# Optimization experiments

Hardware: AMD Instinct MI355X
Metric: run time of the kernel (lower is better)

The kernel has to match this reference:

```python
import jax, jax.numpy as jnp
import numpy as np

EMBED_DIM = 768
NUM_HEADS = 12
HEAD_DIM = EMBED_DIM // NUM_HEADS


def setup_inputs() -> dict:
    key = jax.random.key(0)
    ks = jax.random.split(key, 6)
    B, N = 8, 1024
    x = jax.random.normal(ks[0], (B, N, EMBED_DIM), dtype=jnp.float32)
    pos_embedding = jax.random.normal(ks[1], (1, NUM_HEADS, N, N), dtype=jnp.float32)
    s_in = 1.0 / np.sqrt(EMBED_DIM)
    W_qkv = jax.random.normal(ks[2], (EMBED_DIM, 3 * EMBED_DIM), dtype=jnp.float32) * s_in
    b_qkv = jnp.zeros((3 * EMBED_DIM,), dtype=jnp.float32)
    W_proj = jax.random.normal(ks[3], (EMBED_DIM, EMBED_DIM), dtype=jnp.float32) * s_in
    b_proj = jnp.zeros((EMBED_DIM,), dtype=jnp.float32)
    return {"x": x, "pos_embedding": pos_embedding, "W_qkv": W_qkv,
            "b_qkv": b_qkv, "W_proj": W_proj, "b_proj": b_proj}


def reference(x, pos_embedding, W_qkv, b_qkv, W_proj, b_proj):
    B, N, C = x.shape
    H, D = NUM_HEADS, HEAD_DIM
    qkv = x @ W_qkv + b_qkv                      # [B,N,3C]
    qkv = qkv.reshape(B, N, 3, H, D)
    q = qkv[:, :, 0].transpose(0, 2, 1, 3)       # [B,H,N,D]
    k = qkv[:, :, 1].transpose(0, 2, 1, 3)
    v = qkv[:, :, 2].transpose(0, 2, 1, 3)
    # NOTE: bias is added BEFORE scaling, matching the original module.
    scores = (jnp.einsum('bhnd,bhmd->bhnm', q, k) + pos_embedding) / jnp.sqrt(
        jnp.asarray(D, dtype=x.dtype))
    attn = jax.nn.softmax(scores, axis=-1)       # dropout is identity in eval
    out = jnp.einsum('bhnm,bhmd->bhnd', attn, v)
    out = out.transpose(0, 2, 1, 3).reshape(B, N, C)
    return out @ W_proj + b_proj
```

## Files before the change

kernel.cpp:

```cpp
#include <hip/hip_runtime.h>

#define SEQ   1024
#define HEADS 12
#define CDIM  768
#define BATCH 8

#define QSCALE 0.18033688011112042f

typedef __attribute__((ext_vector_type(8))) short bf16x8;
typedef __attribute__((ext_vector_type(4))) float f32x4;
typedef __attribute__((ext_vector_type(16))) float f32x16;
typedef __attribute__((ext_vector_type(4))) float float4v;
typedef __attribute__((ext_vector_type(4))) short short4v;

__device__ __forceinline__ void gload_lds16(const void* g, void* l) {
  __builtin_amdgcn_global_load_lds(
      (const __attribute__((address_space(1))) unsigned int*)g,
      (__attribute__((address_space(3))) unsigned int*)l, 16, 0, 0);
}

__device__ __forceinline__ unsigned short f2bf(float f) {
  union { float f; unsigned u; } v; v.f = f;
  unsigned r = v.u + 0x7fff + ((v.u >> 16) & 1);
  return (unsigned short)(r >> 16);
}

__device__ __forceinline__ unsigned cvtpk(float a, float b) {
  unsigned r;
  asm("v_cvt_pk_bf16_f32 %0, %1, %2" : "=v"(r) : "v"(a), "v"(b));
  return r;
}

__global__ __launch_bounds__(256) void prep_x_kernel(const float* __restrict__ x,
                                                     short* __restrict__ A) {
  int i = blockIdx.x * 256 + threadIdx.x;
  int r = i / 192;
  int c4 = (i % 192) * 4;
  float4v xv = *(const float4v*)(x + (size_t)r * 768 + c4);
  short4v hi;
#pragma unroll
  for (int j = 0; j < 4; ++j) hi[j] = (short)f2bf(xv[j]);
  *(short4v*)(A + (size_t)r * 768 + c4) = hi;
}

__global__ __launch_bounds__(256) void prep_w_kernel(const float* __restrict__ W,
                                                     short* __restrict__ Bt) {
  __shared__ float tile[64][65];
  int k0 = blockIdx.x * 64;
  int n0 = blockIdx.y * 64;
  int t = threadIdx.x;
#pragma unroll
  for (int it = 0; it < 16; ++it) {
    int r = it * 4 + (t >> 6);
    int c = t & 63;
    tile[r][c] = W[(size_t)(k0 + r) * 2304 + n0 + c];
  }
  __syncthreads();
#pragma unroll
  for (int it = 0; it < 16; ++it) {
    int nr = it * 4 + (t >> 6);
    int kc = t & 63;
    Bt[(size_t)(n0 + nr) * 768 + k0 + kc] = (short)f2bf(tile[kc][nr]);
  }
}

__global__ __launch_bounds__(256) void prep_wp_kernel(const float* __restrict__ W,
                                                      short* __restrict__ Bt) {
  __shared__ float tile[64][65];
  int k0 = blockIdx.x * 64;
  int n0 = blockIdx.y * 64;
  int t = threadIdx.x;
#pragma unroll
  for (int it = 0; it < 16; ++it) {
    int r = it * 4 + (t >> 6);
    int c = t & 63;
    tile[r][c] = W[(size_t)(k0 + r) * 768 + n0 + c];
  }
  __syncthreads();
#pragma unroll
  for (int it = 0; it < 16; ++it) {
    int nr = it * 4 + (t >> 6);
    int kc = t & 63;
    Bt[(size_t)(n0 + nr) * 768 + k0 + kc] = (short)f2bf(tile[kc][nr]);
  }
}

template <int MODE>
__global__ __launch_bounds__(256) void gemm_kernel(
    const short* __restrict__ A, const short* __restrict__ Bt,
    const float* __restrict__ bias,
    short* __restrict__ outQ, short* __restrict__ outK, short* __restrict__ outVT,
    float* __restrict__ outF) {
  const int n0 = blockIdx.x * 128;
  const int m0 = blockIdx.y * 128;
  __shared__ short Als[128 * 64];
  __shared__ short Bls[128 * 64];
  const int tid = threadIdx.x;
  const int lane = tid & 63;
  const int w = tid >> 6;
  const int wr = (w >> 1) * 64;
  const int wc = (w & 1) * 64;
  f32x4 acc[4][4];
#pragma unroll
  for (int mi = 0; mi < 4; ++mi)
#pragma unroll
    for (int ni = 0; ni < 4; ++ni) acc[mi][ni] = (f32x4){0.f, 0.f, 0.f, 0.f};

  for (int k0 = 0; k0 < 768; k0 += 64) {
#pragma unroll
    for (int it = 0; it < 4; ++it) {
      int rbase = it * 32 + w * 8;
      int row = rbase + (lane >> 3);
      int ul = (lane & 7) ^ (row & 7);
      gload_lds16(A + (size_t)(m0 + row) * 768 + k0 + ul * 8, Als + rbase * 64);
      gload_lds16(Bt + (size_t)(n0 + row) * 768 + k0 + ul * 8, Bls + rbase * 64);
    }
    __syncthreads();
#pragma unroll
    for (int kk = 0; kk < 2; ++kk) {
      bf16x8 af[4], bfv[4];
#pragma unroll
      for (int mi = 0; mi < 4; ++mi) {
        int row = wr + mi * 16 + (lane & 15);
        int off = (row * 128 + kk * 64 + (lane >> 4) * 16) ^ ((row & 7) << 4);
        af[mi] = *(const bf16x8*)((const char*)Als + off);
      }
#pragma unroll
      for (int ni = 0; ni < 4; ++ni) {
        int row = wc + ni * 16 + (lane & 15);
        int off = (row * 128 + kk * 64 + (lane >> 4) * 16) ^ ((row & 7) << 4);
        bfv[ni] = *(const bf16x8*)((const char*)Bls + off);
      }
#pragma unroll
      for (int mi = 0; mi < 4; ++mi)
#pragma unroll
        for (int ni = 0; ni < 4; ++ni)
          acc[mi][ni] = __builtin_amdgcn_mfma_f32_16x16x32_bf16(
              af[mi], bfv[ni], acc[mi][ni], 0, 0, 0);
    }
    __syncthreads();
  }
#pragma unroll
  for (int mi = 0; mi < 4; ++mi)
#pragma unroll
    for (int ni = 0; ni < 4; ++ni)
#pragma unroll
      for (int j = 0; j < 4; ++j) {
        int row = m0 + wr + mi * 16 + ((lane >> 4) << 2) + j;
        int col = n0 + wc + ni * 16 + (lane & 15);
        float v = acc[mi][ni][j] + bias[col];
        if (MODE == 1) {
          int three = col / 768;
          int rem = col - three * 768;
          int h = rem >> 6, d = rem & 63;
          int b = row >> 10, n = row & 1023;
          size_t bh = (size_t)(b * 12 + h);
          if (three == 0)      outQ[(bh * 1024 + n) * 64 + d] = (short)f2bf(v * QSCALE);
          else if (three == 1) outK[(bh * 1024 + n) * 64 + d] = (short)f2bf(v);
          else                 outVT[(bh * 64 + d) * 1024 + n] = (short)f2bf(v);
        } else {
          outF[(size_t)row * 768 + col] = v;
        }
      }
}

#define MKFRAG(B, pA, pB, pC, pD)                                    \
  { unsigned x0 = (pA), y0 = (pC), x1 = (pB), y1 = (pD);             \
    asm("v_permlane32_swap_b32 %0, %1" : "+v"(x0), "+v"(y0));        \
    asm("v_permlane32_swap_b32 %0, %1" : "+v"(x1), "+v"(y1));        \
    B.u[0] = x0; B.u[1] = x1; B.u[2] = y0; B.u[3] = y1; }

__global__ __launch_bounds__(256, 3) void attn_kernel(
    const short* __restrict__ qb, const short* __restrict__ kb,
    const short* __restrict__ vtb, const float* __restrict__ pos,
    short* __restrict__ outb) {
  const int bid = blockIdx.x;
  const int lb = (bid & 7) * 96 + (bid >> 3);
  const int qblk = lb & 7;
  const int hb = lb >> 3;
  const int h = hb >> 3, b = hb & 7;

  const int tid = threadIdx.x, lane = tid & 63, w = tid >> 6;
  const int c5 = lane & 31, g1 = lane >> 5;
  const size_t bh = (size_t)(b * 12 + h);
  const short* Q = qb + bh * SEQ * 64;
  const short* K = kb + bh * SEQ * 64;
  const short* VT = vtb + bh * 64 * SEQ;
  const float* Ph = pos + (size_t)h * SEQ * SEQ;
  const int q0w = qblk * 128 + w * 32;

  __shared__ short kls[3 * 4096];
  __shared__ short vls[3 * 4096];

  bf16x8 qf[4];
#pragma unroll
  for (int kd = 0; kd < 4; ++kd)
    qf[kd] = *(const bf16x8*)(Q + (size_t)(q0w + c5) * 64 + kd * 16 + g1 * 8);

  const float* pbase = Ph + (size_t)(q0w + c5) * SEQ + g1 * 4;

  f32x16 o0, o1;
#pragma unroll
  for (int i = 0; i < 16; ++i) { o0[i] = 0.f; o1[i] = 0.f; }
  float lsum = 0.f;

  auto STAGE = [&](short* kb_, short* vb_, int kv0) {
    int r0 = w * 8 + (lane >> 3);
    int u0 = (lane & 7) ^ (r0 & 7);
    gload_lds16(K + (size_t)(kv0 + r0) * 64 + u0 * 8, kb_ + w * 512);
    gload_lds16(K + (size_t)(kv0 + 32 + r0) * 64 + u0 * 8, kb_ + 2048 + w * 512);
    gload_lds16(VT + (size_t)r0 * SEQ + kv0 + u0 * 8, vb_ + w * 512);
    gload_lds16(VT + (size_t)(32 + r0) * SEQ + kv0 + u0 * 8, vb_ + 2048 + w * 512);
  };

  short* kbuf0 = kls;        short* vbuf0 = vls;
  short* kbuf1 = kls + 4096; short* vbuf1 = vls + 4096;
  short* kbuf2 = kls + 8192; short* vbuf2 = vls + 8192;

  STAGE(kbuf0, vbuf0, 0);
  STAGE(kbuf1, vbuf1, 64);
  asm volatile("s_waitcnt vmcnt(4)" ::: "memory");
  __builtin_amdgcn_sched_barrier(0);
  __builtin_amdgcn_s_barrier();

  for (int ti = 0; ti < 16; ++ti) {
    const int kv0 = ti * 64;

    float4v pv0[4], pv1[4];
#pragma unroll
    for (int m = 0; m < 4; ++m) {
      pv0[m] = *(const float4v*)(pbase + kv0 + m * 8);
      pv1[m] = *(const float4v*)(pbase + kv0 + 32 + m * 8);
    }
    asm volatile("" ::: "memory");
    if (ti < 14) STAGE(kbuf2, vbuf2, kv0 + 128);

    const short* kc = kbuf0;
    const short* vc = vbuf0;

    f32x16 p0, p1;
#pragma unroll
    for (int i = 0; i < 16; ++i) { p0[i] = 0.f; p1[i] = 0.f; }
    __builtin_amdgcn_s_setprio(1);
#pragma unroll
    for (int kd = 0; kd < 4; ++kd) {
      int off0 = (c5 * 128 + kd * 32 + g1 * 16) ^ ((c5 & 7) << 4);
      int off1 = ((32 + c5) * 128 + kd * 32 + g1 * 16) ^ ((c5 & 7) << 4);
      bf16x8 kf0 = *(const bf16x8*)((const char*)kc + off0);
      bf16x8 kf1 = *(const bf16x8*)((const char*)kc + off1);
      p0 = __builtin_amdgcn_mfma_f32_32x32x16_bf16(kf0, qf[kd], p0, 0, 0, 0);
      p1 = __builtin_amdgcn_mfma_f32_32x32x16_bf16(kf1, qf[kd], p1, 0, 0, 0);
    }
    __builtin_amdgcn_s_setprio(0);

#pragma unroll
    for (int r = 0; r < 16; ++r) {
      float a = exp2f(fmaf(pv0[r >> 2][r & 3], QSCALE, p0[r]));
      float bq = exp2f(fmaf(pv1[r >> 2][r & 3], QSCALE, p1[r]));
      p0[r] = a; p1[r] = bq;
      lsum += a + bq;
    }

    unsigned pk0[8], pk1[8];
#pragma unroll
    for (int m = 0; m < 4; ++m) {
      pk0[2 * m]     = cvtpk(p0[4 * m],     p0[4 * m + 1]);
      pk0[2 * m + 1] = cvtpk(p0[4 * m + 2], p0[4 * m + 3]);
      pk1[2 * m]     = cvtpk(p1[4 * m],     p1[4 * m + 1]);
      pk1[2 * m + 1] = cvtpk(p1[4 * m + 2], p1[4 * m + 3]);
    }

    union bb { bf16x8 v; unsigned u[4]; } B0, B1, B2, B3;
    MKFRAG(B0, pk0[0], pk0[1], pk0[2], pk0[3]);
    MKFRAG(B1, pk0[4], pk0[5], pk0[6], pk0[7]);
    MKFRAG(B2, pk1[0], pk1[1], pk1[2], pk1[3]);
    MKFRAG(B3, pk1[4], pk1[5], pk1[6], pk1[7]);

    __builtin_amdgcn_s_setprio(1);
#define PVSTEP(Bv, s)                                                        \
    { int o0f = (c5 * 128 + (s) * 32 + g1 * 16) ^ ((c5 & 7) << 4);           \
      int o1f = ((32 + c5) * 128 + (s) * 32 + g1 * 16) ^ ((c5 & 7) << 4);    \
      bf16x8 vf0 = *(const bf16x8*)((const char*)vc + o0f);                  \
      bf16x8 vf1 = *(const bf16x8*)((const char*)vc + o1f);                  \
      o0 = __builtin_amdgcn_mfma_f32_32x32x16_bf16(vf0, Bv.v, o0, 0, 0, 0);  \
      o1 = __builtin_amdgcn_mfma_f32_32x32x16_bf16(vf1, Bv.v, o1, 0, 0, 0); }
    PVSTEP(B0, 0); PVSTEP(B1, 1); PVSTEP(B2, 2); PVSTEP(B3, 3);
#undef PVSTEP
    __builtin_amdgcn_s_setprio(0);

    short* tk = kbuf0; kbuf0 = kbuf1; kbuf1 = kbuf2; kbuf2 = tk;
    short* tv = vbuf0; vbuf0 = vbuf1; vbuf1 = vbuf2; vbuf2 = tv;

    if (ti < 15) {
      if (ti < 14) asm volatile("s_waitcnt vmcnt(4)" ::: "memory");
      else         asm volatile("s_waitcnt vmcnt(0)" ::: "memory");
      __builtin_amdgcn_sched_barrier(0);
      __builtin_amdgcn_s_barrier();
    }
  }

  lsum += __shfl_xor(lsum, 32);
  float inv = 1.0f / lsum;
  size_t obase = (size_t)(b * SEQ + q0w + c5) * 768 + h * 64 + g1 * 4;
#pragma unroll
  for (int m = 0; m < 4; ++m) {
    short4v ov0, ov1;
#pragma unroll
    for (int j = 0; j < 4; ++j) {
      ov0[j] = (short)f2bf(o0[4 * m + j] * inv);
      ov1[j] = (short)f2bf(o1[4 * m + j] * inv);
    }
    *(short4v*)(outb + obase + m * 8) = ov0;
    *(short4v*)(outb + obase + 32 + m * 8) = ov1;
  }
}

extern "C" void kernel_launch(void* const* d_in, const int* in_sizes, int n_in,
                              void* d_out, int out_size, void* d_ws, size_t ws_size,
                              hipStream_t stream) {
  const float* x      = (const float*)d_in[0];
  const float* pos    = (const float*)d_in[1];
  const float* W_qkv  = (const float*)d_in[2];
  const float* b_qkv  = (const float*)d_in[3];
  const float* W_proj = (const float*)d_in[4];
  const float* b_proj = (const float*)d_in[5];
  float* out = (float*)d_out;

  char* ws = (char*)d_ws;
  short* A       = (short*)(ws);
  short* attnbuf = (short*)(ws);
  short* Bt      = (short*)(ws + 12582912);
  short* wpt     = (short*)(ws + 16121856);
  short* qbuf    = (short*)(ws + 17301504);
  short* kbuf    = (short*)(ws + 29884416);
  short* vtbuf   = (short*)(ws + 42467328);

  prep_x_kernel<<<6144, 256, 0, stream>>>(x, A);
  prep_w_kernel<<<dim3(12, 36), 256, 0, stream>>>(W_qkv, Bt);
  prep_wp_kernel<<<dim3(12, 12), 256, 0, stream>>>(W_proj, wpt);
  gemm_kernel<1><<<dim3(18, 64), 256, 0, stream>>>(A, Bt, b_qkv,
                                                   qbuf, kbuf, vtbuf, nullptr);
  attn_kernel<<<768, 256, 0, stream>>>(qbuf, kbuf, vtbuf, pos, attnbuf);
  gemm_kernel<2><<<dim3(6, 64), 256, 0, stream>>>(attnbuf, wpt, b_proj,
                                                  nullptr, nullptr, nullptr, out);
}
```

Measured before the change: 173.3 us.

## Pre-convert pos embedding to prescaled bf16 in attention fragment order

A new prep kernel converts the fp32 positional bias to bf16 once per call. It folds in the softmax scale and stores values in the exact per-lane fragment order the attention kernel consumes. The attention kernel then loads half as many bytes of bias per tile with contiguous 16-byte loads and replaces the fma with an add. This cuts the repeated fp32 bias traffic that every batch re-reads, at the cost of an extra pass over the 50MB tensor and lower bias precision. The QKV GEMM epilogue is also simplified by hoisting the Q/K/V selection out of the per-element loop.

Result: faster. 168.4 us (-2.8%).

```diff
diff --git a/kernel.cpp b/kernel.cpp
--- a/kernel.cpp
+++ b/kernel.cpp
@@ -29,6 +29,12 @@
   unsigned r;
   asm("v_cvt_pk_bf16_f32 %0, %1, %2" : "=v"(r) : "v"(a), "v"(b));
   return r;
+}
+
+__device__ __forceinline__ float bfsel(unsigned u, int odd) {
+  union { unsigned u; float f; } v;
+  v.u = odd ? (u & 0xffff0000u) : (u << 16);
+  return v.f;
 }
 
 __global__ __launch_bounds__(256) void prep_x_kernel(const float* __restrict__ x,
@@ -83,6 +89,31 @@
     int kc = t & 63;
     Bt[(size_t)(n0 + nr) * 768 + k0 + kc] = (short)f2bf(tile[kc][nr]);
   }
+}
+
+__global__ __launch_bounds__(256) void prep_pos_kernel(const float* __restrict__ P,
+                                                       short* __restrict__ PB) {
+  int t = blockIdx.x * 256 + threadIdx.x;
+  int lane = t & 63;
+  int jh   = (t >> 6) & 1;
+  int i0   = (t >> 7) & 1;
+  int w    = (t >> 8) & 3;
+  int ti   = (t >> 10) & 15;
+  int qblk = (t >> 14) & 7;
+  int h    = t >> 17;
+  int c5 = lane & 31, g1 = lane >> 5;
+  int q = qblk * 128 + w * 32 + c5;
+  const float* src = P + ((size_t)h * SEQ + q) * SEQ
+                     + ti * 64 + i0 * 32 + 4 * g1 + 16 * jh;
+  float4v v0 = *(const float4v*)(src);
+  float4v v1 = *(const float4v*)(src + 8);
+  union { short s[8]; bf16x8 v; } o;
+#pragma unroll
+  for (int p = 0; p < 4; ++p) {
+    o.s[p]     = (short)f2bf(v0[p] * QSCALE);
+    o.s[4 + p] = (short)f2bf(v1[p] * QSCALE);
+  }
+  *(bf16x8*)(PB + (size_t)t * 8) = o.v;
 }
 
 template <int MODE>
@@ -140,28 +171,38 @@
     }
     __syncthreads();
   }
-#pragma unroll
-  for (int mi = 0; mi < 4; ++mi)
-#pragma unroll
-    for (int ni = 0; ni < 4; ++ni)
-#pragma unroll
-      for (int j = 0; j < 4; ++j) {
-        int row = m0 + wr + mi * 16 + ((lane >> 4) << 2) + j;
-        int col = n0 + wc + ni * 16 + (lane & 15);
-        float v = acc[mi][ni][j] + bias[col];
-        if (MODE == 1) {
-          int three = col / 768;
-          int rem = col - three * 768;
-          int h = rem >> 6, d = rem & 63;
+  if (MODE == 1) {
+    const int three = n0 / 768;
+    const int nb = n0 - three * 768;
+#pragma unroll
+    for (int mi = 0; mi < 4; ++mi)
+#pragma unroll
+      for (int ni = 0; ni < 4; ++ni)
+#pragma unroll
+        for (int j = 0; j < 4; ++j) {
+          int row = m0 + wr + mi * 16 + ((lane >> 4) << 2) + j;
+          int col = n0 + wc + ni * 16 + (lane & 15);
+          float v = acc[mi][ni][j] + bias[col];
+          int rem = nb + wc + ni * 16 + (lane & 15);
+          int hh = rem >> 6, d = rem & 63;
           int b = row >> 10, n = row & 1023;
-          size_t bh = (size_t)(b * 12 + h);
+          size_t bh = (size_t)(b * 12 + hh);
           if (three == 0)      outQ[(bh * 1024 + n) * 64 + d] = (short)f2bf(v * QSCALE);
           else if (three == 1) outK[(bh * 1024 + n) * 64 + d] = (short)f2bf(v);
           else                 outVT[(bh * 64 + d) * 1024 + n] = (short)f2bf(v);
-        } else {
-          outF[(size_t)row * 768 + col] = v;
         }
-      }
+  } else {
+#pragma unroll
+    for (int mi = 0; mi < 4; ++mi)
+#pragma unroll
+      for (int ni = 0; ni < 4; ++ni)
+#pragma unroll
+        for (int j = 0; j < 4; ++j) {
+          int row = m0 + wr + mi * 16 + ((lane >> 4) << 2) + j;
+          int col = n0 + wc + ni * 16 + (lane & 15);
+          outF[(size_t)row * 768 + col] = acc[mi][ni][j] + bias[col];
+        }
+  }
 }
 
 #define MKFRAG(B, pA, pB, pC, pD)                                    \
@@ -172,7 +213,7 @@
 
 __global__ __launch_bounds__(256, 3) void attn_kernel(
     const short* __restrict__ qb, const short* __restrict__ kb,
-    const short* __restrict__ vtb, const float* __restrict__ pos,
+    const short* __restrict__ vtb, const short* __restrict__ posb,
     short* __restrict__ outb) {
   const int bid = blockIdx.x;
   const int lb = (bid & 7) * 96 + (bid >> 3);
@@ -186,8 +227,10 @@
   const short* Q = qb + bh * SEQ * 64;
   const short* K = kb + bh * SEQ * 64;
   const short* VT = vtb + bh * 64 * SEQ;
-  const float* Ph = pos + (size_t)h * SEQ * SEQ;
   const int q0w = qblk * 128 + w * 32;
+
+  const short* pwb = posb + (size_t)h * 1048576 + (size_t)qblk * 131072
+                     + w * 2048 + lane * 8;
 
   __shared__ short kls[3 * 4096];
   __shared__ short vls[3 * 4096];
@@ -196,8 +239,6 @@
 #pragma unroll
   for (int kd = 0; kd < 4; ++kd)
     qf[kd] = *(const bf16x8*)(Q + (size_t)(q0w + c5) * 64 + kd * 16 + g1 * 8);
-
-  const float* pbase = Ph + (size_t)(q0w + c5) * SEQ + g1 * 4;
 
   f32x16 o0, o1;
 #pragma unroll
@@ -226,12 +267,11 @@
   for (int ti = 0; ti < 16; ++ti) {
     const int kv0 = ti * 64;
 
-    float4v pv0[4], pv1[4];
-#pragma unroll
-    for (int m = 0; m < 4; ++m) {
-      pv0[m] = *(const float4v*)(pbase + kv0 + m * 8);
-      pv1[m] = *(const float4v*)(pbase + kv0 + 32 + m * 8);
-    }
+    union { bf16x8 v; unsigned u[4]; } ua0, ua1, ub0, ub1;
+    ua0.v = *(const bf16x8*)(pwb + ti * 8192);
+    ua1.v = *(const bf16x8*)(pwb + ti * 8192 + 512);
+    ub0.v = *(const bf16x8*)(pwb + ti * 8192 + 1024);
+    ub1.v = *(const bf16x8*)(pwb + ti * 8192 + 1536);
     asm volatile("" ::: "memory");
     if (ti < 14) STAGE(kbuf2, vbuf2, kv0 + 128);
 
@@ -255,8 +295,10 @@
 
 #pragma unroll
     for (int r = 0; r < 16; ++r) {
-      float a = exp2f(fmaf(pv0[r >> 2][r & 3], QSCALE, p0[r]));
-      float bq = exp2f(fmaf(pv1[r >> 2][r & 3], QSCALE, p1[r]));
+      unsigned wa = (r < 8) ? ua0.u[(r >> 1) & 3] : ua1.u[(r >> 1) & 3];
+      unsigned wb = (r < 8) ? ub0.u[(r >> 1) & 3] : ub1.u[(r >> 1) & 3];
+      float a = exp2f(p0[r] + bfsel(wa, r & 1));
+      float bq = exp2f(p1[r] + bfsel(wb, r & 1));
       p0[r] = a; p1[r] = bq;
       lsum += a + bq;
     }
@@ -334,13 +376,15 @@
   short* qbuf    = (short*)(ws + 17301504);
   short* kbuf    = (short*)(ws + 29884416);
   short* vtbuf   = (short*)(ws + 42467328);
+  short* posb    = (short*)(ws + 55050240);
 
   prep_x_kernel<<<6144, 256, 0, stream>>>(x, A);
   prep_w_kernel<<<dim3(12, 36), 256, 0, stream>>>(W_qkv, Bt);
   prep_wp_kernel<<<dim3(12, 12), 256, 0, stream>>>(W_proj, wpt);
+  prep_pos_kernel<<<6144, 256, 0, stream>>>(pos, posb);
   gemm_kernel<1><<<dim3(18, 64), 256, 0, stream>>>(A, Bt, b_qkv,
                                                    qbuf, kbuf, vtbuf, nullptr);
-  attn_kernel<<<768, 256, 0, stream>>>(qbuf, kbuf, vtbuf, pos, attnbuf);
+  attn_kernel<<<768, 256, 0, stream>>>(qbuf, kbuf, vtbuf, posb, attnbuf);
   gemm_kernel<2><<<dim3(6, 64), 256, 0, stream>>>(attnbuf, wpt, b_proj,
                                                   nullptr, nullptr, nullptr, out);
 }
```
